# Kernel tuning notes

Measured on AMD Instinct MI355X. Metric: run time of the kernel, lower is better.

The kernel has to match this reference:

```python
import jax, jax.numpy as jnp
import numpy as np

B = 65536
IN_F = 512
OUT_F = 256
NUM_GROUPS = 8
EPS = 1e-5


def setup_inputs() -> dict:
    key = jax.random.key(0)
    ks = jax.random.split(key, 6)
    return {
        "x": jax.random.normal(ks[0], (B, IN_F), dtype=jnp.float32),
        "weight": jax.random.normal(ks[1], (OUT_F, IN_F), dtype=jnp.float32) * 0.05,
        "bias_linear": jax.random.normal(ks[2], (OUT_F,), dtype=jnp.float32) * 0.05,
        "weight_gn": jax.random.normal(ks[3], (OUT_F,), dtype=jnp.float32),
        "bias_gn": jax.random.normal(ks[4], (OUT_F,), dtype=jnp.float32),
        "bias": jax.random.normal(ks[5], (1, OUT_F, 1, 1), dtype=jnp.float32),
    }


def reference(x, weight, bias_linear, weight_gn, bias_gn, bias):
    # Linear: (B, IN_F) @ (IN_F, OUT_F) + bias -> (B, OUT_F)
    h = jnp.einsum("bi,oi->bo", x, weight) + bias_linear
    # GroupNorm over channel dim (dim=1) with NUM_GROUPS groups
    g = h.reshape(B, NUM_GROUPS, OUT_F // NUM_GROUPS)
    mean = jnp.mean(g, axis=2, keepdims=True)
    var = jnp.mean(jnp.square(g - mean), axis=2, keepdims=True)
    gn = ((g - mean) * jax.lax.rsqrt(var + EPS)).reshape(B, OUT_F)
    gn = gn * weight_gn + bias_gn
    # Min over channels, keepdim -> (B, 1)
    min_vals = jnp.min(gn, axis=1, keepdims=True)
    # torch broadcasting: (B,1) + (1,256,1,1) -> (1,256,B,1)
    result = min_vals + bias
    return result
```

## Files before the change

### kernel.cpp

```cpp
#include <hip/hip_runtime.h>
#include <hip/hip_bf16.h>

#define B_ROWS 65536
#define K_DIM  512
#define N_DIM  256
#define EPS    1e-5f
#define MTILE  32
#define NBLK   256
#define TILES  (B_ROWS / MTILE)
#define STRIDE 520

using short8  = __attribute__((ext_vector_type(8))) short;
using floatx4 = __attribute__((ext_vector_type(4))) float;

#define LBAR() do {                                          \
    __builtin_amdgcn_sched_barrier(0);                       \
    asm volatile("s_waitcnt lgkmcnt(0)" ::: "memory");       \
    __builtin_amdgcn_s_barrier();                            \
    __builtin_amdgcn_sched_barrier(0);                       \
} while (0)

__device__ __forceinline__ unsigned short f2bf(float f) {
    unsigned u = __builtin_bit_cast(unsigned, f);
    u += 0x7FFFu + ((u >> 16) & 1u);
    return (unsigned short)(u >> 16);
}

__global__ __launch_bounds__(64) void pack_w(const float* __restrict__ W,
                                             unsigned short* __restrict__ P) {
    int b    = blockIdx.x;
    int nt   = b >> 4, kk = b & 15;
    int lane = threadIdx.x;
    int l15  = lane & 15, quad = lane >> 4;
    const float* src = W + (size_t)(nt * 16 + l15) * K_DIM + kk * 32 + quad * 8;
    short8 v;
#pragma unroll
    for (int j = 0; j < 8; ++j) v[j] = (short)f2bf(src[j]);
    *(short8*)(P + ((size_t)(nt * 16 + kk) * 64 + lane) * 8) = v;
}

__global__ __launch_bounds__(1024) void fused_persistent(
    const float* __restrict__ X, const unsigned short* __restrict__ P,
    const float* __restrict__ bias_lin, const float* __restrict__ wgn,
    const float* __restrict__ bgn, const float* __restrict__ bias,
    float* __restrict__ out)
{
    __shared__ unsigned short Ash[2][MTILE * STRIDE];
    __shared__ float smS[16][32];
    __shared__ float smSS[16][32];
    __shared__ float smin[16][32];
    __shared__ float m_sh[MTILE];

    const int tid  = threadIdx.x;
    const int wave = tid >> 6;
    const int lane = tid & 63;
    const int l15  = lane & 15, quad = lane >> 4;

    short8 bfr[16];
#pragma unroll
    for (int kkg = 0; kkg < 16; ++kkg)
        bfr[kkg] = *(const short8*)(P + (((size_t)wave * 16 + kkg) * 64 + lane) * 8);

    float blr[4], wgr[4], bgr[4];
#pragma unroll
    for (int r = 0; r < 4; ++r) {
        int c = wave * 16 + quad * 4 + r;
        blr[r] = bias_lin[c]; wgr[r] = wgn[c]; bgr[r] = bgn[c];
    }
    const float bias_c = bias[tid >> 2];

    const int r0 = (tid >> 7) * 4;
    const int c4 = (tid & 127) * 4;

    int t = blockIdx.x;

    float4 xq[4];
#pragma unroll
    for (int p = 0; p < 4; ++p)
        xq[p] = *(const float4*)(X + (size_t)(t * MTILE + r0 + p) * K_DIM + c4);
#pragma unroll
    for (int p = 0; p < 4; ++p) {
        ushort4 h;
        h.x = f2bf(xq[p].x); h.y = f2bf(xq[p].y);
        h.z = f2bf(xq[p].z); h.w = f2bf(xq[p].w);
        *(ushort4*)(&Ash[0][(r0 + p) * STRIDE + c4]) = h;
    }
    if (t + NBLK < TILES) {
#pragma unroll
        for (int p = 0; p < 4; ++p)
            xq[p] = *(const float4*)(X + (size_t)((t + NBLK) * MTILE + r0 + p) * K_DIM + c4);
    }
    LBAR();

    int cur = 0;
    for (; t < TILES; t += NBLK) {
        if (t + NBLK < TILES) {
#pragma unroll
            for (int p = 0; p < 4; ++p) {
                ushort4 h;
                h.x = f2bf(xq[p].x); h.y = f2bf(xq[p].y);
                h.z = f2bf(xq[p].z); h.w = f2bf(xq[p].w);
                *(ushort4*)(&Ash[cur ^ 1][(r0 + p) * STRIDE + c4]) = h;
            }
            if (t + 2 * NBLK < TILES) {
#pragma unroll
                for (int p = 0; p < 4; ++p)
                    xq[p] = *(const float4*)(X + (size_t)((t + 2 * NBLK) * MTILE + r0 + p) * K_DIM + c4);
            }
        }

        floatx4 acc[2];
#pragma unroll
        for (int rt = 0; rt < 2; ++rt)
#pragma unroll
            for (int r = 0; r < 4; ++r) acc[rt][r] = blr[r];
#pragma unroll
        for (int kk = 0; kk < 16; ++kk) {
            short8 a0 = *(const short8*)&Ash[cur][(l15)      * STRIDE + kk * 32 + quad * 8];
            short8 a1 = *(const short8*)&Ash[cur][(16 + l15) * STRIDE + kk * 32 + quad * 8];
            acc[0] = __builtin_amdgcn_mfma_f32_16x16x32_bf16(bfr[kk], a0, acc[0], 0, 0, 0);
            acc[1] = __builtin_amdgcn_mfma_f32_16x16x32_bf16(bfr[kk], a1, acc[1], 0, 0, 0);
        }

        float sreg[2], ssreg[2];
#pragma unroll
        for (int rt = 0; rt < 2; ++rt) {
            float s = 0.f, ss = 0.f;
#pragma unroll
            for (int r = 0; r < 4; ++r) { float v = acc[rt][r]; s += v; ss = fmaf(v, v, ss); }
            s  += __shfl_xor(s, 16);  s  += __shfl_xor(s, 32);
            ss += __shfl_xor(ss, 16); ss += __shfl_xor(ss, 32);
            sreg[rt] = s; ssreg[rt] = ss;
            if (quad == 0) { smS[wave][rt * 16 + l15] = s; smSS[wave][rt * 16 + l15] = ss; }
        }
        LBAR();

#pragma unroll
        for (int rt = 0; rt < 2; ++rt) {
            int row = rt * 16 + l15;
            float st   = sreg[rt]  + smS[wave ^ 1][row];
            float sst  = ssreg[rt] + smSS[wave ^ 1][row];
            float mean = st * (1.0f / 32.0f);
            float var  = sst * (1.0f / 32.0f) - mean * mean;
            float inv  = rsqrtf(var + EPS);
            float mi   = mean * inv;
            float mn   = 1e30f;
#pragma unroll
            for (int r = 0; r < 4; ++r) {
                float g = fmaf(fmaf(acc[rt][r], inv, -mi), wgr[r], bgr[r]);
                mn = fminf(mn, g);
            }
            mn = fminf(mn, __shfl_xor(mn, 16));
            mn = fminf(mn, __shfl_xor(mn, 32));
            if (quad == 0) smin[wave][row] = mn;
        }
        LBAR();

        if (tid < MTILE) {
            float m0 = smin[0][tid];
#pragma unroll
            for (int w = 1; w < 16; ++w) m0 = fminf(m0, smin[w][tid]);
            m_sh[tid] = m0;
        }
        LBAR();

        {
            int c  = tid >> 2;
            int j0 = (tid & 3) * 8;
            float4 ma = *(const float4*)&m_sh[j0];
            float4 mb = *(const float4*)&m_sh[j0 + 4];
            float4 oa, ob;
            oa.x = ma.x + bias_c; oa.y = ma.y + bias_c; oa.z = ma.z + bias_c; oa.w = ma.w + bias_c;
            ob.x = mb.x + bias_c; ob.y = mb.y + bias_c; ob.z = mb.z + bias_c; ob.w = mb.w + bias_c;
            float* dst = out + (size_t)c * B_ROWS + t * MTILE + j0;
            *(float4*)dst       = oa;
            *(float4*)(dst + 4) = ob;
        }
        cur ^= 1;
    }
}

extern "C" void kernel_launch(void* const* d_in, const int* in_sizes, int n_in,
                              void* d_out, int out_size, void* d_ws, size_t ws_size,
                              hipStream_t stream) {
    const float* x    = (const float*)d_in[0];
    const float* w    = (const float*)d_in[1];
    const float* bl   = (const float*)d_in[2];
    const float* wg   = (const float*)d_in[3];
    const float* bg   = (const float*)d_in[4];
    const float* bias = (const float*)d_in[5];

    unsigned short* P = (unsigned short*)d_ws;
    float* out = (float*)d_out;

    hipLaunchKernelGGL(pack_w, dim3(256), dim3(64), 0, stream, w, P);
    hipLaunchKernelGGL(fused_persistent, dim3(NBLK), dim3(1024), 0, stream,
                       x, P, bl, wg, bg, bias, out);
}
```

Baseline: 229.5 us.

## Assign contiguous row chunks per block and batch output stores at the end

```diff
diff --git a/kernel.cpp b/kernel.cpp
--- a/kernel.cpp
+++ b/kernel.cpp
@@ -7,7 +7,8 @@
 #define EPS    1e-5f
 #define MTILE  32
 #define NBLK   256
-#define TILES  (B_ROWS / MTILE)
+#define TPB    8
+#define ROWS_PER_BLK (MTILE * TPB)
 #define STRIDE 520
 
 using short8  = __attribute__((ext_vector_type(8))) short;
@@ -49,7 +50,7 @@
     __shared__ float smS[16][32];
     __shared__ float smSS[16][32];
     __shared__ float smin[16][32];
-    __shared__ float m_sh[MTILE];
+    __shared__ float m_sh[ROWS_PER_BLK];
 
     const int tid  = threadIdx.x;
     const int wave = tid >> 6;
@@ -72,12 +73,12 @@
     const int r0 = (tid >> 7) * 4;
     const int c4 = (tid & 127) * 4;
 
-    int t = blockIdx.x;
+    const size_t row_base = (size_t)blockIdx.x * ROWS_PER_BLK;
 
     float4 xq[4];
 #pragma unroll
     for (int p = 0; p < 4; ++p)
-        xq[p] = *(const float4*)(X + (size_t)(t * MTILE + r0 + p) * K_DIM + c4);
+        xq[p] = *(const float4*)(X + (row_base + r0 + p) * K_DIM + c4);
 #pragma unroll
     for (int p = 0; p < 4; ++p) {
         ushort4 h;
@@ -85,16 +86,14 @@
         h.z = f2bf(xq[p].z); h.w = f2bf(xq[p].w);
         *(ushort4*)(&Ash[0][(r0 + p) * STRIDE + c4]) = h;
     }
-    if (t + NBLK < TILES) {
 #pragma unroll
-        for (int p = 0; p < 4; ++p)
-            xq[p] = *(const float4*)(X + (size_t)((t + NBLK) * MTILE + r0 + p) * K_DIM + c4);
-    }
+    for (int p = 0; p < 4; ++p)
+        xq[p] = *(const float4*)(X + (row_base + MTILE + r0 + p) * K_DIM + c4);
     LBAR();
 
     int cur = 0;
-    for (; t < TILES; t += NBLK) {
-        if (t + NBLK < TILES) {
+    for (int it = 0; it < TPB; ++it) {
+        if (it + 1 < TPB) {
 #pragma unroll
             for (int p = 0; p < 4; ++p) {
                 ushort4 h;
@@ -102,10 +101,10 @@
                 h.z = f2bf(xq[p].z); h.w = f2bf(xq[p].w);
                 *(ushort4*)(&Ash[cur ^ 1][(r0 + p) * STRIDE + c4]) = h;
             }
-            if (t + 2 * NBLK < TILES) {
+            if (it + 2 < TPB) {
 #pragma unroll
                 for (int p = 0; p < 4; ++p)
-                    xq[p] = *(const float4*)(X + (size_t)((t + 2 * NBLK) * MTILE + r0 + p) * K_DIM + c4);
+                    xq[p] = *(const float4*)(X + (row_base + (size_t)(it + 2) * MTILE + r0 + p) * K_DIM + c4);
             }
         }
 
@@ -160,23 +159,24 @@
             float m0 = smin[0][tid];
 #pragma unroll
             for (int w = 1; w < 16; ++w) m0 = fminf(m0, smin[w][tid]);
-            m_sh[tid] = m0;
-        }
-        LBAR();
-
-        {
-            int c  = tid >> 2;
-            int j0 = (tid & 3) * 8;
-            float4 ma = *(const float4*)&m_sh[j0];
-            float4 mb = *(const float4*)&m_sh[j0 + 4];
-            float4 oa, ob;
-            oa.x = ma.x + bias_c; oa.y = ma.y + bias_c; oa.z = ma.z + bias_c; oa.w = ma.w + bias_c;
-            ob.x = mb.x + bias_c; ob.y = mb.y + bias_c; ob.z = mb.z + bias_c; ob.w = mb.w + bias_c;
-            float* dst = out + (size_t)c * B_ROWS + t * MTILE + j0;
-            *(float4*)dst       = oa;
-            *(float4*)(dst + 4) = ob;
+            m_sh[it * MTILE + tid] = m0;
         }
         cur ^= 1;
+    }
+
+    LBAR();
+    {
+        int c = tid >> 2;
+        int q = tid & 3;
+        float* dst = out + (size_t)c * B_ROWS + row_base + q * 64;
+#pragma unroll
+        for (int i = 0; i < 16; ++i) {
+            float4 mv = *(const float4*)&m_sh[q * 64 + i * 4];
+            float4 o;
+            o.x = mv.x + bias_c; o.y = mv.y + bias_c;
+            o.z = mv.z + bias_c; o.w = mv.w + bias_c;
+            *(float4*)(dst + i * 4) = o;
+        }
     }
 }
 
```

Measured after the change: 239.5 us. 4.3% more time.

## Split broadcast output write into separate kernel after fused GEMM-min

Applied to the files above, without the earlier changes.

```diff
diff --git a/kernel.cpp b/kernel.cpp
--- a/kernel.cpp
+++ b/kernel.cpp
@@ -1,5 +1,4 @@
 #include <hip/hip_runtime.h>
-#include <hip/hip_bf16.h>
 
 #define B_ROWS 65536
 #define K_DIM  512
@@ -39,17 +38,15 @@
     *(short8*)(P + ((size_t)(nt * 16 + kk) * 64 + lane) * 8) = v;
 }
 
-__global__ __launch_bounds__(1024) void fused_persistent(
+__global__ __launch_bounds__(1024) void fused_gemm_min(
     const float* __restrict__ X, const unsigned short* __restrict__ P,
     const float* __restrict__ bias_lin, const float* __restrict__ wgn,
-    const float* __restrict__ bgn, const float* __restrict__ bias,
-    float* __restrict__ out)
+    const float* __restrict__ bgn, float* __restrict__ m_out)
 {
     __shared__ unsigned short Ash[2][MTILE * STRIDE];
     __shared__ float smS[16][32];
     __shared__ float smSS[16][32];
     __shared__ float smin[16][32];
-    __shared__ float m_sh[MTILE];
 
     const int tid  = threadIdx.x;
     const int wave = tid >> 6;
@@ -67,7 +64,6 @@
         int c = wave * 16 + quad * 4 + r;
         blr[r] = bias_lin[c]; wgr[r] = wgn[c]; bgr[r] = bgn[c];
     }
-    const float bias_c = bias[tid >> 2];
 
     const int r0 = (tid >> 7) * 4;
     const int c4 = (tid & 127) * 4;
@@ -160,23 +156,29 @@
             float m0 = smin[0][tid];
 #pragma unroll
             for (int w = 1; w < 16; ++w) m0 = fminf(m0, smin[w][tid]);
-            m_sh[tid] = m0;
-        }
-        LBAR();
-
-        {
-            int c  = tid >> 2;
-            int j0 = (tid & 3) * 8;
-            float4 ma = *(const float4*)&m_sh[j0];
-            float4 mb = *(const float4*)&m_sh[j0 + 4];
-            float4 oa, ob;
-            oa.x = ma.x + bias_c; oa.y = ma.y + bias_c; oa.z = ma.z + bias_c; oa.w = ma.w + bias_c;
-            ob.x = mb.x + bias_c; ob.y = mb.y + bias_c; ob.z = mb.z + bias_c; ob.w = mb.w + bias_c;
-            float* dst = out + (size_t)c * B_ROWS + t * MTILE + j0;
-            *(float4*)dst       = oa;
-            *(float4*)(dst + 4) = ob;
+            m_out[t * MTILE + tid] = m0;
         }
         cur ^= 1;
+    }
+}
+
+__global__ __launch_bounds__(256) void bcast_out(
+    const float* __restrict__ m, const float* __restrict__ bias,
+    float* __restrict__ out)
+{
+    const float4* m4  = (const float4*)m;
+    float4*       o4  = (float4*)out;
+    const int bid = blockIdx.x;
+    const int c   = bid >> 3;
+    const float bc = bias[c];
+    const int base = (bid & 7) * 2048;
+#pragma unroll
+    for (int k = 0; k < 8; ++k) {
+        int idx = base + k * 256 + threadIdx.x;
+        float4 mv = m4[idx];
+        float4 o;
+        o.x = mv.x + bc; o.y = mv.y + bc; o.z = mv.z + bc; o.w = mv.w + bc;
+        o4[(size_t)c * (B_ROWS / 4) + idx] = o;
     }
 }
 
@@ -191,9 +193,11 @@
     const float* bias = (const float*)d_in[5];
 
     unsigned short* P = (unsigned short*)d_ws;
-    float* out = (float*)d_out;
+    float* m          = (float*)((char*)d_ws + 262144);
+    float* out        = (float*)d_out;
 
     hipLaunchKernelGGL(pack_w, dim3(256), dim3(64), 0, stream, w, P);
-    hipLaunchKernelGGL(fused_persistent, dim3(NBLK), dim3(1024), 0, stream,
-                       x, P, bl, wg, bg, bias, out);
-}
+    hipLaunchKernelGGL(fused_gemm_min, dim3(NBLK), dim3(1024), 0, stream,
+                       x, P, bl, wg, bg, m);
+    hipLaunchKernelGGL(bcast_out, dim3(2048), dim3(256), 0, stream, m, bias, out);
+}
```

After: 229.7 us. About the same (+0.1%).
